# Kernel optimization log

Hardware: AMD Instinct MI355X
Metric: run time of the kernel (lower is better)

Reference implementation:

```python
import jax, jax.numpy as jnp
import numpy as np

B = 65536
D = 764  # n_dim


def setup_inputs() -> dict:
    key = jax.random.key(0)
    k1, k2, k3 = jax.random.split(key, 3)
    x = jax.random.normal(k1, (B, D), dtype=jnp.float32)
    # Packed weights: row i holds linear_layers[i].weight (length max(1,i), zero-padded).
    W = jax.random.normal(k2, (D, D), dtype=jnp.float32) * 0.02
    b = jax.random.normal(k3, (D,), dtype=jnp.float32) * 0.02
    return {"x": x, "W": W, "b": b}


def reference(x, W, b):
    # Original: output[i] = x[:, :i] @ W_i^T + b_i for i>=1; output[0] = b_0
    # (layer 0 is applied to an explicit zeros tensor, so its weight contributes nothing).
    # This is a single strictly-lower-triangular masked matmul.
    d = W.shape[0]
    mask = jnp.tril(jnp.ones((d, d), dtype=x.dtype), k=-1)  # row i uses cols < i
    return jnp.einsum('bd,nd->bn', x, W * mask) + b  # [B, n_dim]
```

## Files before the change

kernel.cpp:

```cpp
#include <hip/hip_runtime.h>

#define D_DIM 764
#define DP    768
#define BM    128
#define BN    128
#define BK    64

typedef __attribute__((ext_vector_type(8))) short bf16x8;
typedef __attribute__((ext_vector_type(8))) unsigned short u16x8;
typedef __attribute__((ext_vector_type(4))) float f32x4;

typedef __attribute__((address_space(3))) char lds_char;
typedef __attribute__((address_space(1))) const char g_char;

__device__ inline unsigned short f2bf(float f) {
    union { float f; unsigned u; } v; v.f = f;
    unsigned r = v.u + 0x7FFFu + ((v.u >> 16) & 1u);
    return (unsigned short)(r >> 16);
}

__global__ void prep_w(const float* __restrict__ W, unsigned short* __restrict__ Wb) {
    int idx = blockIdx.x * blockDim.x + threadIdx.x;
    int n = idx / DP, k = idx - n * DP;
    float v = 0.0f;
    if (n < D_DIM && k < n) v = W[n * D_DIM + k];
    Wb[idx] = f2bf(v);
}

__global__ __launch_bounds__(512, 4) void fvsbn_gemm(
    const float* __restrict__ X,
    const unsigned short* __restrict__ Wb,
    const float* __restrict__ bias,
    float* __restrict__ out)
{
    __shared__ __align__(16) unsigned short As[2][BM * BK];
    __shared__ __align__(16) unsigned short Bs[3][BN * BK];

    const int tid  = threadIdx.x;
    const int lane = tid & 63;
    const int wid  = tid >> 6;
    const int wm   = wid & 3;
    const int wn   = wid >> 2;
    const int quad = lane >> 4;
    const int l16  = lane & 15;

    const int bid = blockIdx.x;
    const int xcd = bid & 7;
    const int j   = bid >> 3;
    const int nt  = j % 6;
    const int jm  = j / 6;
    const int mt  = jm * 8 + xcd;
    const int m0  = mt * BM;
    const int n0  = nt * BN;

    const int num_k = (n0 + BN) / BK;

    const unsigned short* bsrc[2];
    int bofs[2];
#pragma unroll
    for (int jj = 0; jj < 2; ++jj) {
        const int cbase = (wid * 2 + jj) * 64;
        const int c     = cbase + lane;
        const int r     = c >> 3;
        const int cc    = c & 7;
        const int g     = cc ^ (r & 7);
        bsrc[jj] = Wb + (size_t)(n0 + r) * DP + g * 8;
        bofs[jj] = cbase * 16;
    }

    const float* asrc[2];
    int adst[2], hilim[2];
#pragma unroll
    for (int i = 0; i < 2; ++i) {
        const int p  = tid + i * 512;
        const int r  = p >> 3;
        const int cc = p & 7;
        const int g  = cc ^ (r & 7);
        asrc[i]  = X + (size_t)(m0 + r) * D_DIM + g * 8;
        adst[i]  = r * BK + cc * 8;
        hilim[i] = D_DIM - 8 - g * 8;
    }

    f32x4 acc[2][4];
#pragma unroll
    for (int mi = 0; mi < 2; ++mi)
#pragma unroll
        for (int ni = 0; ni < 4; ++ni) acc[mi][ni] = (f32x4){0.f, 0.f, 0.f, 0.f};

    float4 aLo0[2], aHi0[2], aLo1[2], aHi1[2];

#define STAGE_B(buf, k0s)                                                   \
    _Pragma("unroll")                                                       \
    for (int jj = 0; jj < 2; ++jj)                                          \
        __builtin_amdgcn_global_load_lds((g_char*)(bsrc[jj] + (k0s)),       \
            (lds_char*)((char*)&Bs[0][0] + (buf) * (BN * BK * 2) + bofs[jj]),\
            16, 0, 0);

#define LOAD_A(LO, HI, k0s)                                                 \
    _Pragma("unroll")                                                       \
    for (int i = 0; i < 2; ++i) {                                           \
        const float* lp = asrc[i] + (k0s);                                  \
        LO[i] = *(const float4*)lp;                                         \
        const float* hp = lp + (((k0s) <= hilim[i]) ? 4 : 0);               \
        HI[i] = *(const float4*)hp;  \
    }

#define WRITE_A(LO, HI, abuf)                                               \
    _Pragma("unroll")                                                       \
    for (int i = 0; i < 2; ++i) {                                           \
        u16x8 pk;                                                           \
        pk[0] = f2bf(LO[i].x); pk[1] = f2bf(LO[i].y);                       \
        pk[2] = f2bf(LO[i].z); pk[3] = f2bf(LO[i].w);                       \
        pk[4] = f2bf(HI[i].x); pk[5] = f2bf(HI[i].y);                       \
        pk[6] = f2bf(HI[i].z); pk[7] = f2bf(HI[i].w);                       \
        *(u16x8*)&As[abuf][adst[i]] = pk;                                   \
    }

#define COMPUTE(abuf, bbase)                                                \
    _Pragma("unroll")                                                       \
    for (int s = 0; s < 2; ++s) {                                           \
        bf16x8 af[2], bfr[4];                                               \
        _Pragma("unroll")                                                   \
        for (int mi = 0; mi < 2; ++mi) {                                    \
            const int r = wm * 32 + mi * 16 + l16;                          \
            const int g = s * 4 + quad;                                     \
            af[mi] = *(const bf16x8*)&As[abuf][r * BK + (g ^ (r & 7)) * 8]; \
        }                                                                   \
        _Pragma("unroll")                                                   \
        for (int ni = 0; ni < 4; ++ni) {                                    \
            const int r = wn * 64 + ni * 16 + l16;                          \
            const int g = s * 4 + quad;                                     \
            bfr[ni] = *(const bf16x8*)&(bbase)[r * BK + (g ^ (r & 7)) * 8]; \
        }                                                                   \
        __builtin_amdgcn_s_setprio(1);                                      \
        _Pragma("unroll")                                                   \
        for (int mi = 0; mi < 2; ++mi)                                      \
            _Pragma("unroll")                                               \
            for (int ni = 0; ni < 4; ++ni)                                  \
                acc[mi][ni] = __builtin_amdgcn_mfma_f32_16x16x32_bf16(      \
                    af[mi], bfr[ni], acc[mi][ni], 0, 0, 0);                 \
        __builtin_amdgcn_s_setprio(0);                                      \
    }

    STAGE_B(0, 0);
    LOAD_A(aLo0, aHi0, 0);
    STAGE_B(1, BK);
    LOAD_A(aLo1, aHi1, BK);
    asm volatile("s_waitcnt vmcnt(6)" ::: "memory");
    WRITE_A(aLo0, aHi0, 0);
    asm volatile("s_waitcnt lgkmcnt(0)" ::: "memory");
    __builtin_amdgcn_s_barrier();
    __builtin_amdgcn_sched_barrier(0);

    int bcur = 0;
    for (int t = 0; t < num_k; t += 2) {
        const bool more = (t + 2 < num_k);
        const int  b1   = (bcur == 2) ? 0 : bcur + 1;
        const int  b2   = (bcur == 0) ? 2 : bcur - 1;

        if (more) {
            STAGE_B(b2, (t + 2) * BK);
            LOAD_A(aLo0, aHi0, (t + 2) * BK);
        }
        COMPUTE(0, &As[0][0] == nullptr ? (const unsigned short*)0 : &Bs[bcur][0]);
        if (more) { asm volatile("s_waitcnt vmcnt(6)" ::: "memory"); }
        else      { asm volatile("s_waitcnt vmcnt(0)" ::: "memory"); }
        WRITE_A(aLo1, aHi1, 1);
        asm volatile("s_waitcnt lgkmcnt(0)" ::: "memory");
        __builtin_amdgcn_s_barrier();
        __builtin_amdgcn_sched_barrier(0);

        if (more) {
            STAGE_B(bcur, (t + 3) * BK);
            LOAD_A(aLo1, aHi1, (t + 3) * BK);
        }
        COMPUTE(1, &Bs[b1][0]);
        if (more) {
            asm volatile("s_waitcnt vmcnt(6)" ::: "memory");
            WRITE_A(aLo0, aHi0, 0);
            asm volatile("s_waitcnt lgkmcnt(0)" ::: "memory");
        }
        __builtin_amdgcn_s_barrier();
        __builtin_amdgcn_sched_barrier(0);
        bcur = b2;
    }

#pragma unroll
    for (int ni = 0; ni < 4; ++ni) {
        const int col = n0 + wn * 64 + ni * 16 + l16;
        if (col < D_DIM) {
            const float bv = bias[col];
#pragma unroll
            for (int mi = 0; mi < 2; ++mi) {
                const int row = m0 + wm * 32 + mi * 16 + quad * 4;
#pragma unroll
                for (int r = 0; r < 4; ++r)
                    out[(size_t)(row + r) * D_DIM + col] = acc[mi][ni][r] + bv;
            }
        }
    }
#undef STAGE_B
#undef LOAD_A
#undef WRITE_A
#undef COMPUTE
}

extern "C" void kernel_launch(void* const* d_in, const int* in_sizes, int n_in,
                              void* d_out, int out_size, void* d_ws, size_t ws_size,
                              hipStream_t stream) {
    const float* X    = (const float*)d_in[0];
    const float* W    = (const float*)d_in[1];
    const float* bias = (const float*)d_in[2];
    float* out        = (float*)d_out;
    unsigned short* Wb = (unsigned short*)d_ws;

    prep_w<<<(DP * DP) / 256, 256, 0, stream>>>(W, Wb);
    fvsbn_gemm<<<(65536 / BM) * (DP / BN), 512, 0, stream>>>(X, Wb, bias, out);
}
```

Before: 414.5 us.

## Pre-convert X to bf16 and use LDS-free register-direct MFMA GEMM

Adds a prep pass that converts X to a padded bf16 copy in workspace, then runs a new GEMM kernel that loads MFMA fragments straight from global memory into registers with double buffering and no LDS or barriers. This removes the in-loop fp32-to-bf16 conversion and LDS staging, but adds a full extra read and write pass over X and relies on cache reuse instead of shared tiles. It falls back to the old kernel when the workspace is too small.

```diff
diff --git a/kernel.cpp b/kernel.cpp
--- a/kernel.cpp
+++ b/kernel.cpp
@@ -25,6 +25,104 @@
     float v = 0.0f;
     if (n < D_DIM && k < n) v = W[n * D_DIM + k];
     Wb[idx] = f2bf(v);
+}
+
+__global__ void prep_x(const float* __restrict__ X, unsigned short* __restrict__ Xb) {
+    int idx = blockIdx.x * blockDim.x + threadIdx.x;
+    int r = idx / 96, c = idx - r * 96;
+    const float* xp = X + (size_t)r * D_DIM + c * 8;
+    float4 lo = *(const float4*)xp;
+    float4 hi = (c < 95) ? *(const float4*)(xp + 4)
+                         : make_float4(0.f, 0.f, 0.f, 0.f);
+    u16x8 pk;
+    pk[0] = f2bf(lo.x); pk[1] = f2bf(lo.y); pk[2] = f2bf(lo.z); pk[3] = f2bf(lo.w);
+    pk[4] = f2bf(hi.x); pk[5] = f2bf(hi.y); pk[6] = f2bf(hi.z); pk[7] = f2bf(hi.w);
+    *(u16x8*)&Xb[(size_t)r * DP + c * 8] = pk;
+}
+
+__global__ __launch_bounds__(256) void fvsbn_nolds(
+    const unsigned short* __restrict__ Xb,
+    const unsigned short* __restrict__ Wb,
+    const float* __restrict__ bias,
+    float* __restrict__ out)
+{
+    const int tid  = threadIdx.x;
+    const int lane = tid & 63;
+    const int wid  = tid >> 6;
+    const int wm   = wid & 1;
+    const int wn   = wid >> 1;
+    const int quad = lane >> 4;
+    const int l16  = lane & 15;
+
+    const int bid = blockIdx.x;
+    const int xcd = bid & 7;
+    const int j   = bid >> 3;
+    const int nb  = j % 6;
+    const int jm  = j / 6;
+    const int mb  = jm * 8 + xcd;
+
+    const int m0  = mb * 64 + wm * 32;
+    const int c0  = nb * 128 + wn * 64;
+    const int num_k = (c0 + 64) >> 5;
+
+    const unsigned short* ap = Xb + (size_t)(m0 + l16) * DP + quad * 8;
+    const unsigned short* bp = Wb + (size_t)(c0 + l16) * DP + quad * 8;
+
+    f32x4 acc[2][4];
+#pragma unroll
+    for (int mi = 0; mi < 2; ++mi)
+#pragma unroll
+        for (int ni = 0; ni < 4; ++ni) acc[mi][ni] = (f32x4){0.f, 0.f, 0.f, 0.f};
+
+    bf16x8 a0[2], b0[4], a1[2], b1[4];
+
+#define LOADF(A, Bv, kk)                                                    \
+    {                                                                       \
+        _Pragma("unroll")                                                   \
+        for (int mi = 0; mi < 2; ++mi)                                      \
+            A[mi] = *(const bf16x8*)(ap + mi * 16 * DP + (kk) * 32);        \
+        _Pragma("unroll")                                                   \
+        for (int ni = 0; ni < 4; ++ni)                                      \
+            Bv[ni] = *(const bf16x8*)(bp + ni * 16 * DP + (kk) * 32);       \
+    }
+
+#define MFMAS(A, Bv)                                                        \
+    _Pragma("unroll")                                                       \
+    for (int mi = 0; mi < 2; ++mi)                                          \
+        _Pragma("unroll")                                                   \
+        for (int ni = 0; ni < 4; ++ni)                                      \
+            acc[mi][ni] = __builtin_amdgcn_mfma_f32_16x16x32_bf16(          \
+                A[mi], Bv[ni], acc[mi][ni], 0, 0, 0);
+
+    LOADF(a0, b0, 0);
+    LOADF(a1, b1, 1);
+
+    int kk = 0;
+    for (; kk + 2 < num_k; kk += 2) {
+        MFMAS(a0, b0);
+        LOADF(a0, b0, kk + 2);
+        MFMAS(a1, b1);
+        LOADF(a1, b1, kk + 3);
+    }
+    MFMAS(a0, b0);
+    MFMAS(a1, b1);
+
+#pragma unroll
+    for (int ni = 0; ni < 4; ++ni) {
+        const int col = c0 + ni * 16 + l16;
+        if (col < D_DIM) {
+            const float bv = bias[col];
+#pragma unroll
+            for (int mi = 0; mi < 2; ++mi) {
+                const int row = m0 + mi * 16 + quad * 4;
+#pragma unroll
+                for (int r = 0; r < 4; ++r)
+                    out[(size_t)(row + r) * D_DIM + col] = acc[mi][ni][r] + bv;
+            }
+        }
+    }
+#undef LOADF
+#undef MFMAS
 }
 
 __global__ __launch_bounds__(512, 4) void fvsbn_gemm(
@@ -102,7 +200,7 @@
         const float* lp = asrc[i] + (k0s);                                  \
         LO[i] = *(const float4*)lp;                                         \
         const float* hp = lp + (((k0s) <= hilim[i]) ? 4 : 0);               \
-        HI[i] = *(const float4*)hp;  \
+        HI[i] = *(const float4*)hp;                                         \
     }
 
 #define WRITE_A(LO, HI, abuf)                                               \
@@ -116,7 +214,7 @@
         *(u16x8*)&As[abuf][adst[i]] = pk;                                   \
     }
 
-#define COMPUTE(abuf, bbase)                                                \
+#define COMPUTE(abuf, bbuf)                                                 \
     _Pragma("unroll")                                                       \
     for (int s = 0; s < 2; ++s) {                                           \
         bf16x8 af[2], bfr[4];                                               \
@@ -130,7 +228,7 @@
         for (int ni = 0; ni < 4; ++ni) {                                    \
             const int r = wn * 64 + ni * 16 + l16;                          \
             const int g = s * 4 + quad;                                     \
-            bfr[ni] = *(const bf16x8*)&(bbase)[r * BK + (g ^ (r & 7)) * 8]; \
+            bfr[ni] = *(const bf16x8*)&Bs[bbuf][r * BK + (g ^ (r & 7)) * 8];\
         }                                                                   \
         __builtin_amdgcn_s_setprio(1);                                      \
         _Pragma("unroll")                                                   \
@@ -162,7 +260,7 @@
             STAGE_B(b2, (t + 2) * BK);
             LOAD_A(aLo0, aHi0, (t + 2) * BK);
         }
-        COMPUTE(0, &As[0][0] == nullptr ? (const unsigned short*)0 : &Bs[bcur][0]);
+        COMPUTE(0, bcur);
         if (more) { asm volatile("s_waitcnt vmcnt(6)" ::: "memory"); }
         else      { asm volatile("s_waitcnt vmcnt(0)" ::: "memory"); }
         WRITE_A(aLo1, aHi1, 1);
@@ -174,7 +272,7 @@
             STAGE_B(bcur, (t + 3) * BK);
             LOAD_A(aLo1, aHi1, (t + 3) * BK);
         }
-        COMPUTE(1, &Bs[b1][0]);
+        COMPUTE(1, b1);
         if (more) {
             asm volatile("s_waitcnt vmcnt(6)" ::: "memory");
             WRITE_A(aLo0, aHi0, 0);
@@ -214,6 +312,16 @@
     float* out        = (float*)d_out;
     unsigned short* Wb = (unsigned short*)d_ws;
 
+    const size_t wb_bytes = (size_t)DP * DP * 2;
+    const size_t xb_bytes = (size_t)65536 * DP * 2;
+
     prep_w<<<(DP * DP) / 256, 256, 0, stream>>>(W, Wb);
-    fvsbn_gemm<<<(65536 / BM) * (DP / BN), 512, 0, stream>>>(X, Wb, bias, out);
-}
+
+    if (ws_size >= wb_bytes + xb_bytes) {
+        unsigned short* Xb = (unsigned short*)((char*)d_ws + wb_bytes);
+        prep_x<<<(65536 * 96) / 256, 256, 0, stream>>>(X, Xb);
+        fvsbn_nolds<<<1024 * 6, 256, 0, stream>>>(Xb, Wb, bias, out);
+    } else {
+        fvsbn_gemm<<<(65536 / BM) * (DP / BN), 512, 0, stream>>>(X, Wb, bias, out);
+    }
+}
```

After: 598.7 us. 1.44x slower.
